# Optimization experiments

Hardware: AMD Instinct MI355X
Metric: run time of the kernel (lower is better)

The kernel has to match this reference:

```python
import jax, jax.numpy as jnp
import numpy as np

B, D, H = 512, 256, 512

def setup_inputs() -> dict:
    key = jax.random.key(0)
    ks = jax.random.split(key, 7)
    s = lambda fan_in: 1.0 / np.sqrt(fan_in)
    return {
        "h": jax.random.normal(ks[0], (B, D), jnp.float32),
        "W1": jax.random.normal(ks[1], (2 * D, H), jnp.float32) * s(2 * D),
        "b1": jax.random.normal(ks[2], (H,), jnp.float32) * s(2 * D),
        "W2": jax.random.normal(ks[3], (H, H), jnp.float32) * s(H),
        "b2": jax.random.normal(ks[4], (H,), jnp.float32) * s(H),
        "W3": jax.random.normal(ks[5], (H, 1), jnp.float32) * s(H),
        "b3": jax.random.normal(ks[6], (1,), jnp.float32) * s(H),
    }

def reference(h, W1, b1, W2, b2, W3, b3):
    n = h.shape[0]
    # Split W1 into halves acting on hi and hj; equivalent to cat([hi,hj]) @ W1
    yi = h @ W1[:D]            # [B, H]
    yj = h @ W1[D:]            # [B, H]
    x = jnp.tanh(yi[:, None, :] + yj[None, :, :] + b1)   # [B, B, H]
    x = jnp.tanh(x @ W2 + b2)                             # [B, B, H]
    logits = (x @ W3 + b3)[..., 0]                        # [B, B]
    eye = jnp.eye(n, dtype=logits.dtype)
    return logits * (1.0 - eye) + (-20.0) * eye
```

## Files before the change

### kernel.cpp

```cpp
#include <hip/hip_runtime.h>
#include <cstdint>


#define NB 512
#define ND 256
#define NH 512
#define C2 2.885390081777927f

typedef int i32x4 __attribute__((ext_vector_type(4)));
typedef int i32x16 __attribute__((ext_vector_type(16)));
typedef unsigned int u32;
typedef unsigned char u8;

__device__ __forceinline__ float exp2_fast(float x) {
#if __has_builtin(__builtin_amdgcn_exp2f)
  return __builtin_amdgcn_exp2f(x);
#else
  return exp2f(x);
#endif
}
__device__ __forceinline__ float rcp_fast(float x) {
#if __has_builtin(__builtin_amdgcn_rcpf)
  return __builtin_amdgcn_rcpf(x);
#else
  return 1.0f / x;
#endif
}
__device__ __forceinline__ u32 perm_b32(u32 hi, u32 lo, u32 sel) {
#if __has_builtin(__builtin_amdgcn_perm)
  return __builtin_amdgcn_perm(hi, lo, sel);
#else
  u32 r = 0;
  for (int b = 0; b < 4; ++b) {
    const u32 c = (sel >> (8 * b)) & 255;
    const u32 byte = (c < 4) ? (lo >> (8 * c)) & 255 : (c < 8) ? (hi >> (8 * (c - 4))) & 255 : 0;
    r |= byte << (8 * b);
  }
  return r;
#endif
}
__device__ __forceinline__ u32 tanh_q127_magic(float u) {
  const float r = rcp_fast(exp2_fast(u) + 1.0f);
  return __builtin_bit_cast(u32, fmaf(-254.0f, r, 12583039.0f));
}

__device__ __forceinline__ uint4 pack16(const float4* fa, const float4* ga) {
  u32 wds[4];
#pragma unroll
  for (int q = 0; q < 4; ++q) {
    const u32 m0 = tanh_q127_magic(fa[q].x + ga[q].x);
    const u32 m1 = tanh_q127_magic(fa[q].y + ga[q].y);
    const u32 m2 = tanh_q127_magic(fa[q].z + ga[q].z);
    const u32 m3 = tanh_q127_magic(fa[q].w + ga[q].w);
    const u32 p01 = perm_b32(m1, m0, 0x0C0C0400u);
    const u32 p23 = perm_b32(m3, m2, 0x0C0C0400u);
    wds[q] = perm_b32(p23, p01, 0x05040100u);
  }
  return make_uint4(wds[0], wds[1], wds[2], wds[3]);
}

__global__ __launch_bounds__(256) void prep_all(const float* __restrict__ h,
                                                const float* __restrict__ W1,
                                                const float* __restrict__ b1,
                                                const float* __restrict__ W2,
                                                float* __restrict__ Ai,
                                                float* __restrict__ Aj,
                                                u8* __restrict__ W2q) {
  const int t = threadIdx.x;
  const int bx = blockIdx.x;
  if (bx < 256) {
    __shared__ float hsh[4][ND];
    const int i0 = (bx >> 1) * 4;
    const int n = (bx & 1) * 256 + t;
#pragma unroll
    for (int ii = 0; ii < 4; ++ii) hsh[ii][t] = h[(i0 + ii) * ND + t];
    __syncthreads();
    float ai[4] = {0.0f, 0.0f, 0.0f, 0.0f};
    float aj[4] = {0.0f, 0.0f, 0.0f, 0.0f};
#pragma unroll 4
    for (int d = 0; d < ND; ++d) {
      const float wa = W1[d * NH + n];
      const float wb = W1[(d + ND) * NH + n];
#pragma unroll
      for (int ii = 0; ii < 4; ++ii) {
        const float hd = hsh[ii][d];
        ai[ii] = fmaf(hd, wa, ai[ii]);
        aj[ii] = fmaf(hd, wb, aj[ii]);
      }
    }
    const float b1n = b1[n];
#pragma unroll
    for (int ii = 0; ii < 4; ++ii) {
      Ai[(i0 + ii) * NH + n] = ai[ii] * C2;
      Aj[(i0 + ii) * NH + n] = (aj[ii] + b1n) * C2;
    }
  } else {
    const int g = (bx - 256) * 256 + t;
    const int lane = g & 63;
    const int nt = (g >> 6) & 15;
    const int ks = g >> 10;
    const int n = nt * 32 + (lane & 31);
    const int kb = ks * 32 + ((lane >> 5) << 4);
    u32 w[4];
#pragma unroll
    for (int q = 0; q < 4; ++q) {
      u32 acc = 0;
#pragma unroll
      for (int j = 0; j < 4; ++j) {
        const float wv = fminf(fmaxf(W2[(kb + q * 4 + j) * NH + n], -0.25f), 0.25f);
        const int qi = (int)rintf(wv * 508.0f);
        acc |= ((u32)(qi & 255)) << (8 * j);
      }
      w[q] = acc;
    }
    ((uint4*)W2q)[g] = make_uint4(w[0], w[1], w[2], w[3]);
  }
}

__global__ __launch_bounds__(512, 2) void pair_main(const float* __restrict__ Ai,
                                                    const float* __restrict__ Aj,
                                                    const u8* __restrict__ W2q,
                                                    const float* __restrict__ b2,
                                                    const float* __restrict__ W3,
                                                    const float* __restrict__ b3,
                                                    float* __restrict__ out) {
  __shared__ __align__(16) u8 xs[2][32 * 512];
  __shared__ float red[2][8][32];

  const int t = threadIdx.x;
  const int w = t >> 6;
  const int lane = t & 63;
  const int lhi = lane >> 5;
  const int llo = lane & 31;
  const int bx = blockIdx.x;
  const int jt = bx & 15;
  const int ich = bx >> 4;
  const int j0 = jt * 32;
  const int i0 = ich * 32;

  i32x4 Bf[16][2];
  {
    const uint4* w2v = (const uint4*)W2q + w * 128 + lane;
#pragma unroll
    for (int ks = 0; ks < 16; ++ks) {
      Bf[ks][0] = __builtin_bit_cast(i32x4, w2v[ks * 1024]);
      Bf[ks][1] = __builtin_bit_cast(i32x4, w2v[ks * 1024 + 64]);
    }
  }

  const float SCALE = (0.25f / (127.0f * 127.0f)) * C2;
  float b2c[2], w3v[2];
#pragma unroll
  for (int ntl = 0; ntl < 2; ++ntl) {
    const int n = w * 64 + ntl * 32 + llo;
    b2c[ntl] = b2[n] * C2;
    w3v[ntl] = W3[n];
  }
  float w3s = w3v[0] + w3v[1];
#pragma unroll
  for (int off = 1; off < 32; off <<= 1) w3s += __shfl_xor(w3s, off, 64);
  const float b3v = b3[0];

  const int srow = t & 31;
  const int ss0 = t >> 5;
  const int k0 = ss0 * 16;

  float4 fj[8];
  {
    const float* ajr = Aj + (size_t)(j0 + srow) * NH;
#pragma unroll
    for (int q = 0; q < 4; ++q) {
      fj[q] = *(const float4*)(ajr + k0 + q * 4);
      fj[q + 4] = *(const float4*)(ajr + k0 + 256 + q * 4);
    }
  }

  {
    const float* air = Ai + (size_t)i0 * NH;
    float4 gi[8];
#pragma unroll
    for (int q = 0; q < 4; ++q) {
      gi[q] = *(const float4*)(air + k0 + q * 4);
      gi[q + 4] = *(const float4*)(air + k0 + 256 + q * 4);
    }
    ((uint4*)xs[0])[ss0 * 32 + srow] = pack16(fj, gi);
    ((uint4*)xs[0])[(ss0 + 16) * 32 + srow] = pack16(fj + 4, gi + 4);
  }
  __syncthreads();

  const int abase = lhi * 32 + llo;

  for (int il = 0; il < 32; ++il) {
    const int buf = il & 1;
    const int i = i0 + il;

    float4 gi[8];
    if (il < 31) {
      const float* air = Ai + (size_t)(i + 1) * NH;
#pragma unroll
      for (int q = 0; q < 4; ++q) {
        gi[q] = *(const float4*)(air + k0 + q * 4);
        gi[q + 4] = *(const float4*)(air + k0 + 256 + q * 4);
      }
    }

    i32x16 acc[2];
#pragma unroll
    for (int ntl = 0; ntl < 2; ++ntl)
#pragma unroll
      for (int q = 0; q < 16; ++q) acc[ntl][q] = 0;
    {
      const i32x4* xv = (const i32x4*)(xs[buf]);
#pragma unroll
      for (int ks = 0; ks < 16; ++ks) {
        const i32x4 a = xv[ks * 64 + abase];
        acc[0] = __builtin_amdgcn_mfma_i32_32x32x32_i8(a, Bf[ks][0], acc[0], 0, 0, 0);
        acc[1] = __builtin_amdgcn_mfma_i32_32x32x32_i8(a, Bf[ks][1], acc[1], 0, 0, 0);
      }
    }

    if (il < 31) {
      ((uint4*)xs[buf ^ 1])[ss0 * 32 + srow] = pack16(fj, gi);
      ((uint4*)xs[buf ^ 1])[(ss0 + 16) * 32 + srow] = pack16(fj + 4, gi + 4);
    }

#pragma unroll
    for (int reg = 0; reg < 16; ++reg) {
      float sr = 0.0f;
#pragma unroll
      for (int ntl = 0; ntl < 2; ++ntl) {
        const float y = fmaf((float)acc[ntl][reg], SCALE, b2c[ntl]);
        const float r = rcp_fast(exp2_fast(y) + 1.0f);
        sr = fmaf(w3v[ntl], r, sr);
      }
#pragma unroll
      for (int off = 1; off < 32; off <<= 1) sr += __shfl_xor(sr, off, 64);
      const int row = (reg & 3) + 8 * (reg >> 2) + 4 * lhi;
      if (llo == reg) red[buf][w][row] = fmaf(-2.0f, sr, w3s);
    }

    if (il > 0 && t < 32) {
      float v = b3v;
#pragma unroll
      for (int ww = 0; ww < 8; ++ww) v += red[buf ^ 1][ww][t];
      const int ip = i - 1;
      const int j = j0 + t;
      out[ip * NB + j] = (j == ip) ? -20.0f : v;
    }

    __syncthreads();
  }

  if (t < 32) {
    float v = b3v;
#pragma unroll
    for (int ww = 0; ww < 8; ++ww) v += red[1][ww][t];
    const int ip = i0 + 31;
    const int j = j0 + t;
    out[ip * NB + j] = (j == ip) ? -20.0f : v;
  }
}

extern "C" void kernel_launch(void* const* d_in, const int* in_sizes, int n_in,
                              void* d_out, int out_size, void* d_ws, size_t ws_size,
                              hipStream_t stream) {
  const float* h = (const float*)d_in[0];
  const float* W1 = (const float*)d_in[1];
  const float* b1 = (const float*)d_in[2];
  const float* W2 = (const float*)d_in[3];
  const float* b2 = (const float*)d_in[4];
  const float* W3 = (const float*)d_in[5];
  const float* b3 = (const float*)d_in[6];
  float* out = (float*)d_out;

  float* Ai = (float*)d_ws;
  float* Aj = Ai + NB * NH;
  u8* W2q = (u8*)(Aj + NB * NH);

  prep_all<<<320, 256, 0, stream>>>(h, W1, b1, W2, Ai, Aj, W2q);
  pair_main<<<256, 512, 0, stream>>>(Ai, Aj, W2q, b2, W3, b3, out);
}
```

Before: 267.6 us.

## Split pair kernel into small 2-row blocks streaming W2 from global memory

Replaces the 256-block persistent loop, where each block held W2 fragments in registers and iterated over 32 rows of i, with 4096 short blocks. Each block handles 2 i rows by 32 j columns and streams the quantized W2 fragments from global or L2 with a two-deep register prefetch. Occupancy is raised to 4 blocks per CU. This trades W2 register residency and reuse for far more parallelism and lower register pressure, but every block now reloads all of W2 (256 KB) and redoes the setup and tanh packing.

```diff
diff --git a/kernel.cpp b/kernel.cpp
--- a/kernel.cpp
+++ b/kernel.cpp
@@ -42,21 +42,6 @@
 __device__ __forceinline__ u32 tanh_q127_magic(float u) {
   const float r = rcp_fast(exp2_fast(u) + 1.0f);
   return __builtin_bit_cast(u32, fmaf(-254.0f, r, 12583039.0f));
-}
-
-__device__ __forceinline__ uint4 pack16(const float4* fa, const float4* ga) {
-  u32 wds[4];
-#pragma unroll
-  for (int q = 0; q < 4; ++q) {
-    const u32 m0 = tanh_q127_magic(fa[q].x + ga[q].x);
-    const u32 m1 = tanh_q127_magic(fa[q].y + ga[q].y);
-    const u32 m2 = tanh_q127_magic(fa[q].z + ga[q].z);
-    const u32 m3 = tanh_q127_magic(fa[q].w + ga[q].w);
-    const u32 p01 = perm_b32(m1, m0, 0x0C0C0400u);
-    const u32 p23 = perm_b32(m3, m2, 0x0C0C0400u);
-    wds[q] = perm_b32(p23, p01, 0x05040100u);
-  }
-  return make_uint4(wds[0], wds[1], wds[2], wds[3]);
 }
 
 __global__ __launch_bounds__(256) void prep_all(const float* __restrict__ h,
@@ -117,7 +102,7 @@
   }
 }
 
-__global__ __launch_bounds__(512, 2) void pair_main(const float* __restrict__ Ai,
+__global__ __launch_bounds__(512, 4) void pair_main(const float* __restrict__ Ai,
                                                     const float* __restrict__ Aj,
                                                     const u8* __restrict__ W2q,
                                                     const float* __restrict__ b2,
@@ -126,6 +111,7 @@
                                                     float* __restrict__ out) {
   __shared__ __align__(16) u8 xs[2][32 * 512];
   __shared__ float red[2][8][32];
+  __shared__ float wsum[8];
 
   const int t = threadIdx.x;
   const int w = t >> 6;
@@ -133,20 +119,8 @@
   const int lhi = lane >> 5;
   const int llo = lane & 31;
   const int bx = blockIdx.x;
-  const int jt = bx & 15;
-  const int ich = bx >> 4;
-  const int j0 = jt * 32;
-  const int i0 = ich * 32;
-
-  i32x4 Bf[16][2];
-  {
-    const uint4* w2v = (const uint4*)W2q + w * 128 + lane;
-#pragma unroll
-    for (int ks = 0; ks < 16; ++ks) {
-      Bf[ks][0] = __builtin_bit_cast(i32x4, w2v[ks * 1024]);
-      Bf[ks][1] = __builtin_bit_cast(i32x4, w2v[ks * 1024 + 64]);
-    }
-  }
+  const int i0 = (bx >> 4) * 2;
+  const int j0 = (bx & 15) * 32;
 
   const float SCALE = (0.25f / (127.0f * 127.0f)) * C2;
   float b2c[2], w3v[2];
@@ -156,108 +130,128 @@
     b2c[ntl] = b2[n] * C2;
     w3v[ntl] = W3[n];
   }
-  float w3s = w3v[0] + w3v[1];
-#pragma unroll
-  for (int off = 1; off < 32; off <<= 1) w3s += __shfl_xor(w3s, off, 64);
-  const float b3v = b3[0];
-
-  const int srow = t & 31;
-  const int ss0 = t >> 5;
-  const int k0 = ss0 * 16;
-
-  float4 fj[8];
   {
+    float w3s = w3v[0] + w3v[1];
+#pragma unroll
+    for (int off = 1; off < 32; off <<= 1) w3s += __shfl_xor(w3s, off, 64);
+    if (lane == 0) wsum[w] = w3s;
+  }
+
+  {
+    const int srow = t & 31;
+    const int ss0 = t >> 5;
+    const int k0 = ss0 * 16;
     const float* ajr = Aj + (size_t)(j0 + srow) * NH;
-#pragma unroll
-    for (int q = 0; q < 4; ++q) {
-      fj[q] = *(const float4*)(ajr + k0 + q * 4);
-      fj[q + 4] = *(const float4*)(ajr + k0 + 256 + q * 4);
-    }
-  }
+    const float* air0 = Ai + (size_t)i0 * NH;
+    const float* air1 = Ai + (size_t)(i0 + 1) * NH;
+    u32 wd0[8], wd1[8];
+#pragma unroll
+    for (int g = 0; g < 8; ++g) {
+      const int ko = k0 + (g & 3) * 4 + (g >> 2) * 256;
+      const float4 fa = *(const float4*)(ajr + ko);
+      const float4 g0 = *(const float4*)(air0 + ko);
+      const float4 g1 = *(const float4*)(air1 + ko);
+      {
+        const u32 m0 = tanh_q127_magic(fa.x + g0.x);
+        const u32 m1 = tanh_q127_magic(fa.y + g0.y);
+        const u32 m2 = tanh_q127_magic(fa.z + g0.z);
+        const u32 m3 = tanh_q127_magic(fa.w + g0.w);
+        const u32 p01 = perm_b32(m1, m0, 0x0C0C0400u);
+        const u32 p23 = perm_b32(m3, m2, 0x0C0C0400u);
+        wd0[g] = perm_b32(p23, p01, 0x05040100u);
+      }
+      {
+        const u32 m0 = tanh_q127_magic(fa.x + g1.x);
+        const u32 m1 = tanh_q127_magic(fa.y + g1.y);
+        const u32 m2 = tanh_q127_magic(fa.z + g1.z);
+        const u32 m3 = tanh_q127_magic(fa.w + g1.w);
+        const u32 p01 = perm_b32(m1, m0, 0x0C0C0400u);
+        const u32 p23 = perm_b32(m3, m2, 0x0C0C0400u);
+        wd1[g] = perm_b32(p23, p01, 0x05040100u);
+      }
+    }
+    ((uint4*)xs[0])[ss0 * 32 + srow] = make_uint4(wd0[0], wd0[1], wd0[2], wd0[3]);
+    ((uint4*)xs[0])[(ss0 + 16) * 32 + srow] = make_uint4(wd0[4], wd0[5], wd0[6], wd0[7]);
+    ((uint4*)xs[1])[ss0 * 32 + srow] = make_uint4(wd1[0], wd1[1], wd1[2], wd1[3]);
+    ((uint4*)xs[1])[(ss0 + 16) * 32 + srow] = make_uint4(wd1[4], wd1[5], wd1[6], wd1[7]);
+  }
+  __syncthreads();
+
+  i32x16 acc[2][2];
+#pragma unroll
+  for (int ii = 0; ii < 2; ++ii)
+#pragma unroll
+    for (int nt = 0; nt < 2; ++nt)
+#pragma unroll
+      for (int q = 0; q < 16; ++q) acc[ii][nt][q] = 0;
 
   {
-    const float* air = Ai + (size_t)i0 * NH;
-    float4 gi[8];
-#pragma unroll
-    for (int q = 0; q < 4; ++q) {
-      gi[q] = *(const float4*)(air + k0 + q * 4);
-      gi[q + 4] = *(const float4*)(air + k0 + 256 + q * 4);
-    }
-    ((uint4*)xs[0])[ss0 * 32 + srow] = pack16(fj, gi);
-    ((uint4*)xs[0])[(ss0 + 16) * 32 + srow] = pack16(fj + 4, gi + 4);
-  }
-  __syncthreads();
-
-  const int abase = lhi * 32 + llo;
-
-  for (int il = 0; il < 32; ++il) {
-    const int buf = il & 1;
-    const int i = i0 + il;
-
-    float4 gi[8];
-    if (il < 31) {
-      const float* air = Ai + (size_t)(i + 1) * NH;
-#pragma unroll
-      for (int q = 0; q < 4; ++q) {
-        gi[q] = *(const float4*)(air + k0 + q * 4);
-        gi[q + 4] = *(const float4*)(air + k0 + 256 + q * 4);
-      }
-    }
-
-    i32x16 acc[2];
-#pragma unroll
-    for (int ntl = 0; ntl < 2; ++ntl)
-#pragma unroll
-      for (int q = 0; q < 16; ++q) acc[ntl][q] = 0;
-    {
-      const i32x4* xv = (const i32x4*)(xs[buf]);
-#pragma unroll
-      for (int ks = 0; ks < 16; ++ks) {
-        const i32x4 a = xv[ks * 64 + abase];
-        acc[0] = __builtin_amdgcn_mfma_i32_32x32x32_i8(a, Bf[ks][0], acc[0], 0, 0, 0);
-        acc[1] = __builtin_amdgcn_mfma_i32_32x32x32_i8(a, Bf[ks][1], acc[1], 0, 0, 0);
-      }
-    }
-
-    if (il < 31) {
-      ((uint4*)xs[buf ^ 1])[ss0 * 32 + srow] = pack16(fj, gi);
-      ((uint4*)xs[buf ^ 1])[(ss0 + 16) * 32 + srow] = pack16(fj + 4, gi + 4);
-    }
-
+    const i32x4* xv0 = (const i32x4*)xs[0];
+    const i32x4* xv1 = (const i32x4*)xs[1];
+    const int abase = lhi * 32 + llo;
+    const uint4* w2v = (const uint4*)W2q + w * 128 + lane;
+
+    i32x4 a0[2], a1[2];
+    uint4 b0[2], b1[2];
+    a0[0] = xv0[abase];
+    a1[0] = xv1[abase];
+    a0[1] = xv0[64 + abase];
+    a1[1] = xv1[64 + abase];
+    b0[0] = w2v[0];
+    b1[0] = w2v[64];
+    b0[1] = w2v[1024];
+    b1[1] = w2v[1024 + 64];
+
+#pragma unroll
+    for (int ks = 0; ks < 16; ++ks) {
+      const int p = ks & 1;
+      const i32x4 aa0 = a0[p];
+      const i32x4 aa1 = a1[p];
+      const i32x4 c0 = __builtin_bit_cast(i32x4, b0[p]);
+      const i32x4 c1 = __builtin_bit_cast(i32x4, b1[p]);
+      if (ks < 14) {
+        a0[p] = xv0[(ks + 2) * 64 + abase];
+        a1[p] = xv1[(ks + 2) * 64 + abase];
+        const uint4* wp = w2v + (ks + 2) * 1024;
+        b0[p] = wp[0];
+        b1[p] = wp[64];
+      }
+      acc[0][0] = __builtin_amdgcn_mfma_i32_32x32x32_i8(aa0, c0, acc[0][0], 0, 0, 0);
+      acc[0][1] = __builtin_amdgcn_mfma_i32_32x32x32_i8(aa0, c1, acc[0][1], 0, 0, 0);
+      acc[1][0] = __builtin_amdgcn_mfma_i32_32x32x32_i8(aa1, c0, acc[1][0], 0, 0, 0);
+      acc[1][1] = __builtin_amdgcn_mfma_i32_32x32x32_i8(aa1, c1, acc[1][1], 0, 0, 0);
+    }
+  }
+
+#pragma unroll
+  for (int ii = 0; ii < 2; ++ii) {
 #pragma unroll
     for (int reg = 0; reg < 16; ++reg) {
       float sr = 0.0f;
 #pragma unroll
       for (int ntl = 0; ntl < 2; ++ntl) {
-        const float y = fmaf((float)acc[ntl][reg], SCALE, b2c[ntl]);
+        const float y = fmaf((float)acc[ii][ntl][reg], SCALE, b2c[ntl]);
         const float r = rcp_fast(exp2_fast(y) + 1.0f);
         sr = fmaf(w3v[ntl], r, sr);
       }
 #pragma unroll
       for (int off = 1; off < 32; off <<= 1) sr += __shfl_xor(sr, off, 64);
       const int row = (reg & 3) + 8 * (reg >> 2) + 4 * lhi;
-      if (llo == reg) red[buf][w][row] = fmaf(-2.0f, sr, w3s);
-    }
-
-    if (il > 0 && t < 32) {
-      float v = b3v;
-#pragma unroll
-      for (int ww = 0; ww < 8; ++ww) v += red[buf ^ 1][ww][t];
-      const int ip = i - 1;
-      const int j = j0 + t;
-      out[ip * NB + j] = (j == ip) ? -20.0f : v;
-    }
-
-    __syncthreads();
-  }
-
-  if (t < 32) {
-    float v = b3v;
-#pragma unroll
-    for (int ww = 0; ww < 8; ++ww) v += red[1][ww][t];
-    const int ip = i0 + 31;
-    const int j = j0 + t;
-    out[ip * NB + j] = (j == ip) ? -20.0f : v;
+      if (llo == reg) red[ii][w][row] = -2.0f * sr;
+    }
+  }
+  __syncthreads();
+
+  if (t < 64) {
+    const int ii = t >> 5;
+    const int row = t & 31;
+    float v = b3[0] + ((wsum[0] + wsum[1]) + (wsum[2] + wsum[3])) +
+              ((wsum[4] + wsum[5]) + (wsum[6] + wsum[7]));
+#pragma unroll
+    for (int ww = 0; ww < 8; ++ww) v += red[ii][ww][row];
+    const int icur = i0 + ii;
+    const int j = j0 + row;
+    out[icur * NB + j] = (j == icur) ? -20.0f : v;
   }
 }
 
@@ -278,5 +272,5 @@
   u8* W2q = (u8*)(Aj + NB * NH);
 
   prep_all<<<320, 256, 0, stream>>>(h, W1, b1, W2, Ai, Aj, W2q);
-  pair_main<<<256, 512, 0, stream>>>(Ai, Aj, W2q, b2, W3, b3, out);
-}
+  pair_main<<<4096, 512, 0, stream>>>(Ai, Aj, W2q, b2, W3, b3, out);
+}
```

New measurement: 236.4 us. -11.7%, faster.
